# Kernel optimization log

Hardware: AMD Instinct MI355X
Metric: run time of the kernel (lower is better)

Reference implementation:

```python
import jax, jax.numpy as jnp
import numpy as np

S = 2048      # seq len (q and kv)
D_MODEL = 2048
H = 16        # num heads
HD = D_MODEL // H  # head dim = 128


def softmax1(x):
    # off-by-one softmax: denominator has extra exp(-m) term (the '1' = e^0 shifted by max)
    m = jnp.maximum(jax.lax.stop_gradient(x.max(-1, keepdims=True)), 0)
    un = jnp.exp(x - m)
    return un / (jnp.exp(-m) + jnp.sum(un, axis=-1, keepdims=True))


def setup_inputs() -> dict:
    key = jax.random.key(0)
    ks = jax.random.split(key, 8)
    std = 1.0 / np.sqrt(D_MODEL)
    return {
        "query": jax.random.normal(ks[0], (S, D_MODEL), jnp.float32),
        "key_": jax.random.normal(ks[1], (S, D_MODEL), jnp.float32),
        "value": jax.random.normal(ks[2], (S, D_MODEL), jnp.float32),
        "Wq": jax.random.uniform(ks[3], (D_MODEL, D_MODEL), jnp.float32, -std, std),
        "Wk": jax.random.uniform(ks[4], (D_MODEL, D_MODEL), jnp.float32, -std, std),
        "Wv": jax.random.uniform(ks[5], (D_MODEL, D_MODEL), jnp.float32, -std, std),
        "Wo": jax.random.uniform(ks[6], (D_MODEL, D_MODEL), jnp.float32, -std, std),
        "scalars": jnp.ones((H,), jnp.float32),
    }


def reference(query, key_, value, Wq, Wk, Wv, Wo, scalars):
    # equinox Linear: y = W @ x, weight shape (out, in), no bias
    qh = (query @ Wq.T).reshape(S, H, HD)   # [S, H, HD]
    kh = (key_ @ Wk.T).reshape(S, H, HD)
    vh = (value @ Wv.T).reshape(S, H, HD)
    scale = 1.0 / jnp.sqrt(jnp.asarray(HD, qh.dtype))
    logits = jnp.einsum("qhd,khd->hqk", qh * scale, kh)  # [H, S, S]
    w = softmax1(logits)
    attn = jnp.einsum("hqk,khd->qhd", w, vh)             # [S, H, HD]
    attn = attn * scalars[None, :, None]
    return attn.reshape(S, H * HD) @ Wo.T                # [S, D_MODEL]
```

## Files before the change

kernel.cpp:

```cpp
#include <hip/hip_runtime.h>
#include <hip/hip_bf16.h>


#define S_LEN 2048
#define DMODEL 2048
#define NHEAD 16
#define HEADD 128

typedef __bf16 bf16x8 __attribute__((ext_vector_type(8)));
typedef __bf16 bf16x4 __attribute__((ext_vector_type(4)));
typedef float f32x4 __attribute__((ext_vector_type(4)));

__device__ inline void async_copy16(const __bf16* g, __bf16* l) {
    __builtin_amdgcn_global_load_lds(
        (const __attribute__((address_space(1))) unsigned int*)g,
        (__attribute__((address_space(3))) unsigned int*)l, 16, 0, 0);
}

__global__ __launch_bounds__(256) void conv2(const float* __restrict__ s0,
                                             __hip_bfloat16* __restrict__ h0,
                                             __hip_bfloat16* __restrict__ l0,
                                             float sc0,
                                             const float* __restrict__ s1,
                                             __hip_bfloat16* __restrict__ h1,
                                             __hip_bfloat16* __restrict__ l1,
                                             float sc1) {
    const float* s = blockIdx.y ? s1 : s0;
    __hip_bfloat16* ph = blockIdx.y ? h1 : h0;
    __hip_bfloat16* pl = blockIdx.y ? l1 : l0;
    const float sc = blockIdx.y ? sc1 : sc0;
    size_t i4 = (size_t)blockIdx.x * 256 + threadIdx.x;
    float4 v = *(const float4*)&s[i4 * 4];
    float x0 = v.x * sc, x1 = v.y * sc, x2 = v.z * sc, x3 = v.w * sc;
    bf16x4 hv, lv;
    __bf16 a0 = (__bf16)x0, a1 = (__bf16)x1, a2 = (__bf16)x2, a3 = (__bf16)x3;
    hv[0] = a0; hv[1] = a1; hv[2] = a2; hv[3] = a3;
    lv[0] = (__bf16)(x0 - (float)a0); lv[1] = (__bf16)(x1 - (float)a1);
    lv[2] = (__bf16)(x2 - (float)a2); lv[3] = (__bf16)(x3 - (float)a3);
    *(bf16x4*)&ph[i4 * 4] = hv;
    *(bf16x4*)&pl[i4 * 4] = lv;
}

template <int OUTMODE>
__global__ __launch_bounds__(256) void gemm_nt3(const __bf16* __restrict__ Ahi,
                                                const __bf16* __restrict__ Alo,
                                                const __bf16* __restrict__ Bhi,
                                                const __bf16* __restrict__ Blo,
                                                float* __restrict__ Cf,
                                                __hip_bfloat16* __restrict__ Chi,
                                                __hip_bfloat16* __restrict__ Clo) {
    constexpr int K = DMODEL, N = DMODEL;
    __shared__ __bf16 sAhi[128 * 32], sAlo[128 * 32];
    __shared__ __bf16 sBhi[64 * 32], sBlo[64 * 32];

    const int tid = threadIdx.x;
    const int lane = tid & 63;
    const int wave = tid >> 6;
    const int qr = lane & 15;
    const int quad = lane >> 4;
    const int wm = (wave >> 1) * 64;
    const int wn = (wave & 1) * 32;
    const size_t row0 = (size_t)blockIdx.y * 128;
    const size_t col0 = (size_t)blockIdx.x * 64;

    const int arow = tid >> 2, acol = (tid & 3) * 8;
    const __bf16* gAh = Ahi + (row0 + arow) * K + acol;
    const __bf16* gAh2 = gAh + (size_t)64 * K;
    const __bf16* gAl = Alo + (row0 + arow) * K + acol;
    const __bf16* gAl2 = gAl + (size_t)64 * K;
    const __bf16* gBh = Bhi + (col0 + arow) * K + acol;
    const __bf16* gBl = Blo + (col0 + arow) * K + acol;
    __bf16* lAh = sAhi + tid * 8;
    __bf16* lAh2 = sAhi + tid * 8 + 2048;
    __bf16* lAl = sAlo + tid * 8;
    __bf16* lAl2 = sAlo + tid * 8 + 2048;
    __bf16* lBh = sBhi + tid * 8;
    __bf16* lBl = sBlo + tid * 8;

    f32x4 acc[4][2] = {};

    for (int k0 = 0; k0 < K; k0 += 32) {
        async_copy16(gAh, lAh);
        async_copy16(gAh2, lAh2);
        async_copy16(gAl, lAl);
        async_copy16(gAl2, lAl2);
        async_copy16(gBh, lBh);
        async_copy16(gBl, lBl);
        gAh += 32; gAh2 += 32; gAl += 32; gAl2 += 32; gBh += 32; gBl += 32;
        __syncthreads();

        bf16x8 a_h[4], a_l[4], b_h[2], b_l[2];
#pragma unroll
        for (int i = 0; i < 4; ++i) {
            a_h[i] = *(const bf16x8*)&sAhi[(wm + i * 16 + qr) * 32 + quad * 8];
            a_l[i] = *(const bf16x8*)&sAlo[(wm + i * 16 + qr) * 32 + quad * 8];
        }
#pragma unroll
        for (int j = 0; j < 2; ++j) {
            b_h[j] = *(const bf16x8*)&sBhi[(wn + j * 16 + qr) * 32 + quad * 8];
            b_l[j] = *(const bf16x8*)&sBlo[(wn + j * 16 + qr) * 32 + quad * 8];
        }
#pragma unroll
        for (int i = 0; i < 4; ++i)
#pragma unroll
            for (int j = 0; j < 2; ++j) {
                acc[i][j] = __builtin_amdgcn_mfma_f32_16x16x32_bf16(a_h[i], b_h[j], acc[i][j], 0, 0, 0);
                acc[i][j] = __builtin_amdgcn_mfma_f32_16x16x32_bf16(a_h[i], b_l[j], acc[i][j], 0, 0, 0);
                acc[i][j] = __builtin_amdgcn_mfma_f32_16x16x32_bf16(a_l[i], b_h[j], acc[i][j], 0, 0, 0);
            }
        __syncthreads();
    }

#pragma unroll
    for (int i = 0; i < 4; ++i)
#pragma unroll
        for (int j = 0; j < 2; ++j)
#pragma unroll
            for (int r = 0; r < 4; ++r) {
                size_t idx = (row0 + wm + i * 16 + quad * 4 + r) * N +
                             col0 + wn + j * 16 + qr;
                float x = acc[i][j][r];
                if (OUTMODE == 0) {
                    Cf[idx] = x;
                } else if (OUTMODE == 1) {
                    Chi[idx] = __float2bfloat16(x);
                } else {
                    __bf16 hv = (__bf16)x;
                    Chi[idx] = *(__hip_bfloat16*)&hv;
                    __bf16 lv = (__bf16)(x - (float)hv);
                    Clo[idx] = *(__hip_bfloat16*)&lv;
                }
            }
}

__global__ __launch_bounds__(256) void attn_mfma(const __bf16* __restrict__ qhi_g,
                                                 const __bf16* __restrict__ qlo_g,
                                                 const __bf16* __restrict__ khi_g,
                                                 const __bf16* __restrict__ klo_g,
                                                 const __bf16* __restrict__ vhT,
                                                 const float* __restrict__ scalars,
                                                 __bf16* __restrict__ ohi_g,
                                                 __bf16* __restrict__ olo_g) {
    const int h = blockIdx.y;
    const int q0 = blockIdx.x * 64;
    __shared__ __align__(16) __bf16 Khi[64][136];
    __shared__ __align__(16) __bf16 Klo[64][136];
    __shared__ __align__(16) __bf16 VT[128][72];
    __shared__ __align__(16) __bf16 Ps[64][72];

    const int tid = threadIdx.x;
    const int lane = tid & 63;
    const int wave = tid >> 6;
    const int qr = lane & 15;
    const int quad = lane >> 4;

    bf16x8 qfh[4], qfl[4];
    {
        const __bf16* qrh = qhi_g + (size_t)(q0 + wave * 16 + qr) * DMODEL + h * HEADD;
        const __bf16* qrl = qlo_g + (size_t)(q0 + wave * 16 + qr) * DMODEL + h * HEADD;
#pragma unroll
        for (int kc = 0; kc < 4; ++kc) {
            qfh[kc] = *(const bf16x8*)&qrh[kc * 32 + quad * 8];
            qfl[kc] = *(const bf16x8*)&qrl[kc * 32 + quad * 8];
        }
    }

    f32x4 oacc[8] = {};
    float m_r[4], l_r[4];
#pragma unroll
    for (int r = 0; r < 4; ++r) { m_r[r] = 0.f; l_r[r] = 1.f; }

    for (int k0 = 0; k0 < S_LEN; k0 += 64) {
#pragma unroll
        for (int i = 0; i < 4; ++i) {
            int idx = tid + i * 256;
            int kp = idx >> 4;
            int c8 = (idx & 15) * 8;
            size_t goff = (size_t)(k0 + kp) * DMODEL + h * HEADD + c8;
            *(bf16x8*)&Khi[kp][c8] = *(const bf16x8*)&khi_g[goff];
            *(bf16x8*)&Klo[kp][c8] = *(const bf16x8*)&klo_g[goff];
        }
#pragma unroll
        for (int i = 0; i < 4; ++i) {
            int idx = tid + i * 256;
            int dm = idx >> 3;
            int c8 = (idx & 7) * 8;
            *(bf16x8*)&VT[dm][c8] =
                *(const bf16x8*)&vhT[(size_t)(h * HEADD + dm) * S_LEN + k0 + c8];
        }
        __syncthreads();

        f32x4 S[4] = {};
#pragma unroll
        for (int jt = 0; jt < 4; ++jt) {
#pragma unroll
            for (int kc = 0; kc < 4; ++kc) {
                bf16x8 kh8 = *(const bf16x8*)&Khi[jt * 16 + qr][kc * 32 + quad * 8];
                bf16x8 kl8 = *(const bf16x8*)&Klo[jt * 16 + qr][kc * 32 + quad * 8];
                S[jt] = __builtin_amdgcn_mfma_f32_16x16x32_bf16(qfh[kc], kh8, S[jt], 0, 0, 0);
                S[jt] = __builtin_amdgcn_mfma_f32_16x16x32_bf16(qfh[kc], kl8, S[jt], 0, 0, 0);
                S[jt] = __builtin_amdgcn_mfma_f32_16x16x32_bf16(qfl[kc], kh8, S[jt], 0, 0, 0);
            }
        }

#pragma unroll
        for (int r = 0; r < 4; ++r) {
            float mx = fmaxf(fmaxf(S[0][r], S[1][r]), fmaxf(S[2][r], S[3][r]));
#pragma unroll
            for (int m = 1; m < 16; m <<= 1) mx = fmaxf(mx, __shfl_xor(mx, m, 64));
            float m_new = fmaxf(m_r[r], mx);
            float alpha = __expf(m_r[r] - m_new);
            float sum = 0.f;
            int prow = wave * 16 + quad * 4 + r;
#pragma unroll
            for (int jt = 0; jt < 4; ++jt) {
                float e = __expf(S[jt][r] - m_new);
                sum += e;
                Ps[prow][jt * 16 + qr] = (__bf16)e;
            }
#pragma unroll
            for (int m = 1; m < 16; m <<= 1) sum += __shfl_xor(sum, m, 64);
            l_r[r] = l_r[r] * alpha + sum;
            m_r[r] = m_new;
#pragma unroll
            for (int nt = 0; nt < 8; ++nt) oacc[nt][r] *= alpha;
        }
        __syncthreads();

#pragma unroll
        for (int kc = 0; kc < 2; ++kc) {
            bf16x8 pf = *(const bf16x8*)&Ps[wave * 16 + qr][kc * 32 + quad * 8];
#pragma unroll
            for (int nt = 0; nt < 8; ++nt) {
                bf16x8 vf = *(const bf16x8*)&VT[nt * 16 + qr][kc * 32 + quad * 8];
                oacc[nt] = __builtin_amdgcn_mfma_f32_16x16x32_bf16(pf, vf, oacc[nt], 0, 0, 0);
            }
        }
        __syncthreads();
    }

    const float sh = scalars[h];
#pragma unroll
    for (int r = 0; r < 4; ++r) {
        float wm = sh / l_r[r];
        size_t rowoff = (size_t)(q0 + wave * 16 + quad * 4 + r) * DMODEL + h * HEADD;
#pragma unroll
        for (int nt = 0; nt < 8; ++nt) {
            float x = oacc[nt][r] * wm;
            __bf16 hv = (__bf16)x;
            ohi_g[rowoff + nt * 16 + qr] = hv;
            olo_g[rowoff + nt * 16 + qr] = (__bf16)(x - (float)hv);
        }
    }
}

extern "C" void kernel_launch(void* const* d_in, const int* in_sizes, int n_in,
                              void* d_out, int out_size, void* d_ws, size_t ws_size,
                              hipStream_t stream) {
    const float* query   = (const float*)d_in[0];
    const float* key_    = (const float*)d_in[1];
    const float* value   = (const float*)d_in[2];
    const float* Wq      = (const float*)d_in[3];
    const float* Wk      = (const float*)d_in[4];
    const float* Wv      = (const float*)d_in[5];
    const float* Wo      = (const float*)d_in[6];
    const float* scalars = (const float*)d_in[7];
    float* out = (float*)d_out;

    const size_t PL = (size_t)S_LEN * DMODEL;
    __bf16* P = (__bf16*)d_ws;
    __bf16* pa_hi = P;
    __bf16* pa_lo = P + PL;
    __bf16* pb_hi = P + 2 * PL;
    __bf16* pb_lo = P + 3 * PL;
    __bf16* qh_hi = P + 4 * PL;
    __bf16* qh_lo = P + 5 * PL;
    __bf16* kh_hi = P + 6 * PL;
    __bf16* kh_lo = P + 7 * PL;
    __bf16* vhT   = P + 8 * PL;

    const float scale = 0.08838834764831844f;
    dim3 cg(2048 * 2048 / 4 / 256, 2), cb(256);
    dim3 gg(DMODEL / 64, S_LEN / 128), gb(256);

#define CONV(sA, scA, sB, scB)                                                   \
    conv2<<<cg, cb, 0, stream>>>(sA, (__hip_bfloat16*)pa_hi, (__hip_bfloat16*)pa_lo, scA, \
                                 sB, (__hip_bfloat16*)pb_hi, (__hip_bfloat16*)pb_lo, scB)

    CONV(query, 1.0f, Wq, scale);
    gemm_nt3<2><<<gg, gb, 0, stream>>>(pa_hi, pa_lo, pb_hi, pb_lo,
                                       nullptr, (__hip_bfloat16*)qh_hi, (__hip_bfloat16*)qh_lo);
    CONV(key_, 1.0f, Wk, 1.0f);
    gemm_nt3<2><<<gg, gb, 0, stream>>>(pa_hi, pa_lo, pb_hi, pb_lo,
                                       nullptr, (__hip_bfloat16*)kh_hi, (__hip_bfloat16*)kh_lo);
    CONV(Wv, 1.0f, value, 1.0f);
    gemm_nt3<1><<<gg, gb, 0, stream>>>(pa_hi, pa_lo, pb_hi, pb_lo,
                                       nullptr, (__hip_bfloat16*)vhT, nullptr);

    attn_mfma<<<dim3(S_LEN / 64, NHEAD), 256, 0, stream>>>(
        qh_hi, qh_lo, kh_hi, kh_lo, vhT, scalars, qh_hi, qh_lo);

    conv2<<<dim3(2048 * 2048 / 4 / 256, 1), cb, 0, stream>>>(
        Wo, (__hip_bfloat16*)pb_hi, (__hip_bfloat16*)pb_lo, 1.0f,
        Wo, (__hip_bfloat16*)pb_hi, (__hip_bfloat16*)pb_lo, 1.0f);
    gemm_nt3<0><<<gg, gb, 0, stream>>>(qh_hi, qh_lo, pb_hi, pb_lo,
                                       out, nullptr, nullptr);
#undef CONV
}
```

Measured before the change: 574.1 us.

## Enlarge per-wave GEMM tile and batch Q/K projections into one launch

```diff
diff --git a/kernel.cpp b/kernel.cpp
--- a/kernel.cpp
+++ b/kernel.cpp
@@ -41,69 +41,65 @@
     *(bf16x4*)&pl[i4 * 4] = lv;
 }
 
+struct GArgs {
+    const __bf16 *Ah, *Al, *Bh, *Bl;
+    float* Cf;
+    __bf16 *Ch, *Cl;
+};
+
 template <int OUTMODE>
-__global__ __launch_bounds__(256) void gemm_nt3(const __bf16* __restrict__ Ahi,
-                                                const __bf16* __restrict__ Alo,
-                                                const __bf16* __restrict__ Bhi,
-                                                const __bf16* __restrict__ Blo,
-                                                float* __restrict__ Cf,
-                                                __hip_bfloat16* __restrict__ Chi,
-                                                __hip_bfloat16* __restrict__ Clo) {
+__global__ __launch_bounds__(128, 3) void gemm_nt3(GArgs g0, GArgs g1) {
     constexpr int K = DMODEL, N = DMODEL;
-    __shared__ __bf16 sAhi[128 * 32], sAlo[128 * 32];
-    __shared__ __bf16 sBhi[64 * 32], sBlo[64 * 32];
+    const GArgs g = blockIdx.z ? g1 : g0;
+    __shared__ __bf16 sAh[128 * 32], sAl[128 * 32];
+    __shared__ __bf16 sBh[64 * 32], sBl[64 * 32];
 
     const int tid = threadIdx.x;
     const int lane = tid & 63;
     const int wave = tid >> 6;
     const int qr = lane & 15;
     const int quad = lane >> 4;
-    const int wm = (wave >> 1) * 64;
-    const int wn = (wave & 1) * 32;
     const size_t row0 = (size_t)blockIdx.y * 128;
     const size_t col0 = (size_t)blockIdx.x * 64;
 
-    const int arow = tid >> 2, acol = (tid & 3) * 8;
-    const __bf16* gAh = Ahi + (row0 + arow) * K + acol;
-    const __bf16* gAh2 = gAh + (size_t)64 * K;
-    const __bf16* gAl = Alo + (row0 + arow) * K + acol;
-    const __bf16* gAl2 = gAl + (size_t)64 * K;
-    const __bf16* gBh = Bhi + (col0 + arow) * K + acol;
-    const __bf16* gBl = Blo + (col0 + arow) * K + acol;
-    __bf16* lAh = sAhi + tid * 8;
-    __bf16* lAh2 = sAhi + tid * 8 + 2048;
-    __bf16* lAl = sAlo + tid * 8;
-    __bf16* lAl2 = sAlo + tid * 8 + 2048;
-    __bf16* lBh = sBhi + tid * 8;
-    __bf16* lBl = sBlo + tid * 8;
-
-    f32x4 acc[4][2] = {};
+    const int srow = tid >> 2;
+    const int k8 = (tid & 3) * 8;
+    const __bf16* gAh = g.Ah + (row0 + srow) * K + k8;
+    const __bf16* gAl = g.Al + (row0 + srow) * K + k8;
+    const __bf16* gBh = g.Bh + (col0 + srow) * K + k8;
+    const __bf16* gBl = g.Bl + (col0 + srow) * K + k8;
+
+    f32x4 acc[4][4] = {};
 
     for (int k0 = 0; k0 < K; k0 += 32) {
-        async_copy16(gAh, lAh);
-        async_copy16(gAh2, lAh2);
-        async_copy16(gAl, lAl);
-        async_copy16(gAl2, lAl2);
-        async_copy16(gBh, lBh);
-        async_copy16(gBl, lBl);
-        gAh += 32; gAh2 += 32; gAl += 32; gAl2 += 32; gBh += 32; gBl += 32;
-        __syncthreads();
-
-        bf16x8 a_h[4], a_l[4], b_h[2], b_l[2];
+#pragma unroll
+        for (int c = 0; c < 4; ++c) {
+            async_copy16(gAh + (size_t)c * 32 * K, sAh + c * 1024 + tid * 8);
+            async_copy16(gAl + (size_t)c * 32 * K, sAl + c * 1024 + tid * 8);
+        }
+#pragma unroll
+        for (int c = 0; c < 2; ++c) {
+            async_copy16(gBh + (size_t)c * 32 * K, sBh + c * 1024 + tid * 8);
+            async_copy16(gBl + (size_t)c * 32 * K, sBl + c * 1024 + tid * 8);
+        }
+        gAh += 32; gAl += 32; gBh += 32; gBl += 32;
+        __syncthreads();
+
+        bf16x8 a_h[4], a_l[4], b_h[4], b_l[4];
 #pragma unroll
         for (int i = 0; i < 4; ++i) {
-            a_h[i] = *(const bf16x8*)&sAhi[(wm + i * 16 + qr) * 32 + quad * 8];
-            a_l[i] = *(const bf16x8*)&sAlo[(wm + i * 16 + qr) * 32 + quad * 8];
-        }
-#pragma unroll
-        for (int j = 0; j < 2; ++j) {
-            b_h[j] = *(const bf16x8*)&sBhi[(wn + j * 16 + qr) * 32 + quad * 8];
-            b_l[j] = *(const bf16x8*)&sBlo[(wn + j * 16 + qr) * 32 + quad * 8];
+            a_h[i] = *(const bf16x8*)&sAh[(wave * 64 + i * 16 + qr) * 32 + quad * 8];
+            a_l[i] = *(const bf16x8*)&sAl[(wave * 64 + i * 16 + qr) * 32 + quad * 8];
+        }
+#pragma unroll
+        for (int j = 0; j < 4; ++j) {
+            b_h[j] = *(const bf16x8*)&sBh[(j * 16 + qr) * 32 + quad * 8];
+            b_l[j] = *(const bf16x8*)&sBl[(j * 16 + qr) * 32 + quad * 8];
         }
 #pragma unroll
         for (int i = 0; i < 4; ++i)
 #pragma unroll
-            for (int j = 0; j < 2; ++j) {
+            for (int j = 0; j < 4; ++j) {
                 acc[i][j] = __builtin_amdgcn_mfma_f32_16x16x32_bf16(a_h[i], b_h[j], acc[i][j], 0, 0, 0);
                 acc[i][j] = __builtin_amdgcn_mfma_f32_16x16x32_bf16(a_h[i], b_l[j], acc[i][j], 0, 0, 0);
                 acc[i][j] = __builtin_amdgcn_mfma_f32_16x16x32_bf16(a_l[i], b_h[j], acc[i][j], 0, 0, 0);
@@ -114,21 +110,20 @@
 #pragma unroll
     for (int i = 0; i < 4; ++i)
 #pragma unroll
-        for (int j = 0; j < 2; ++j)
+        for (int j = 0; j < 4; ++j)
 #pragma unroll
             for (int r = 0; r < 4; ++r) {
-                size_t idx = (row0 + wm + i * 16 + quad * 4 + r) * N +
-                             col0 + wn + j * 16 + qr;
+                size_t idx = (row0 + wave * 64 + i * 16 + quad * 4 + r) * N +
+                             col0 + j * 16 + qr;
                 float x = acc[i][j][r];
                 if (OUTMODE == 0) {
-                    Cf[idx] = x;
+                    g.Cf[idx] = x;
                 } else if (OUTMODE == 1) {
-                    Chi[idx] = __float2bfloat16(x);
+                    g.Ch[idx] = (__bf16)x;
                 } else {
                     __bf16 hv = (__bf16)x;
-                    Chi[idx] = *(__hip_bfloat16*)&hv;
-                    __bf16 lv = (__bf16)(x - (float)hv);
-                    Clo[idx] = *(__hip_bfloat16*)&lv;
+                    g.Ch[idx] = hv;
+                    g.Cl[idx] = (__bf16)(x - (float)hv);
                 }
             }
 }
@@ -268,42 +263,39 @@
     float* out = (float*)d_out;
 
     const size_t PL = (size_t)S_LEN * DMODEL;
-    __bf16* P = (__bf16*)d_ws;
-    __bf16* pa_hi = P;
-    __bf16* pa_lo = P + PL;
-    __bf16* pb_hi = P + 2 * PL;
-    __bf16* pb_lo = P + 3 * PL;
-    __bf16* qh_hi = P + 4 * PL;
-    __bf16* qh_lo = P + 5 * PL;
-    __bf16* kh_hi = P + 6 * PL;
-    __bf16* kh_lo = P + 7 * PL;
-    __bf16* vhT   = P + 8 * PL;
+    __bf16* p[12];
+    for (int i = 0; i < 12; ++i) p[i] = (__bf16*)d_ws + i * PL;
 
     const float scale = 0.08838834764831844f;
     dim3 cg(2048 * 2048 / 4 / 256, 2), cb(256);
-    dim3 gg(DMODEL / 64, S_LEN / 128), gb(256);
-
-#define CONV(sA, scA, sB, scB)                                                   \
-    conv2<<<cg, cb, 0, stream>>>(sA, (__hip_bfloat16*)pa_hi, (__hip_bfloat16*)pa_lo, scA, \
-                                 sB, (__hip_bfloat16*)pb_hi, (__hip_bfloat16*)pb_lo, scB)
-
-    CONV(query, 1.0f, Wq, scale);
-    gemm_nt3<2><<<gg, gb, 0, stream>>>(pa_hi, pa_lo, pb_hi, pb_lo,
-                                       nullptr, (__hip_bfloat16*)qh_hi, (__hip_bfloat16*)qh_lo);
-    CONV(key_, 1.0f, Wk, 1.0f);
-    gemm_nt3<2><<<gg, gb, 0, stream>>>(pa_hi, pa_lo, pb_hi, pb_lo,
-                                       nullptr, (__hip_bfloat16*)kh_hi, (__hip_bfloat16*)kh_lo);
-    CONV(Wv, 1.0f, value, 1.0f);
-    gemm_nt3<1><<<gg, gb, 0, stream>>>(pa_hi, pa_lo, pb_hi, pb_lo,
-                                       nullptr, (__hip_bfloat16*)vhT, nullptr);
+    dim3 gg(DMODEL / 64, S_LEN / 128, 1), gb(128);
+    dim3 gg2(DMODEL / 64, S_LEN / 128, 2);
+
+#define BH(x) (__hip_bfloat16*)(x)
+    conv2<<<cg, cb, 0, stream>>>(query, BH(p[0]), BH(p[1]), 1.0f,
+                                 Wq, BH(p[2]), BH(p[3]), scale);
+    conv2<<<cg, cb, 0, stream>>>(key_, BH(p[4]), BH(p[5]), 1.0f,
+                                 Wk, BH(p[6]), BH(p[7]), 1.0f);
+    {
+        GArgs gq = {p[0], p[1], p[2], p[3], nullptr, p[8], p[9]};
+        GArgs gk = {p[4], p[5], p[6], p[7], nullptr, p[10], p[11]};
+        gemm_nt3<2><<<gg2, gb, 0, stream>>>(gq, gk);
+    }
+    conv2<<<cg, cb, 0, stream>>>(Wv, BH(p[0]), BH(p[1]), 1.0f,
+                                 value, BH(p[2]), BH(p[3]), 1.0f);
+    {
+        GArgs gv = {p[0], p[1], p[2], p[3], nullptr, p[4], nullptr};
+        gemm_nt3<1><<<gg, gb, 0, stream>>>(gv, gv);
+    }
 
     attn_mfma<<<dim3(S_LEN / 64, NHEAD), 256, 0, stream>>>(
-        qh_hi, qh_lo, kh_hi, kh_lo, vhT, scalars, qh_hi, qh_lo);
+        p[8], p[9], p[10], p[11], p[4], scalars, p[8], p[9]);
 
     conv2<<<dim3(2048 * 2048 / 4 / 256, 1), cb, 0, stream>>>(
-        Wo, (__hip_bfloat16*)pb_hi, (__hip_bfloat16*)pb_lo, 1.0f,
-        Wo, (__hip_bfloat16*)pb_hi, (__hip_bfloat16*)pb_lo, 1.0f);
-    gemm_nt3<0><<<gg, gb, 0, stream>>>(qh_hi, qh_lo, pb_hi, pb_lo,
-                                       out, nullptr, nullptr);
-#undef CONV
-}
+        Wo, BH(p[0]), BH(p[1]), 1.0f, Wo, BH(p[0]), BH(p[1]), 1.0f);
+    {
+        GArgs go = {p[8], p[9], p[0], p[1], out, nullptr, nullptr};
+        gemm_nt3<0><<<gg, gb, 0, stream>>>(go, go);
+    }
+#undef BH
+}
```

Measured after the change: 566.1 us. About the same (-1.4%).
